# Performance work log

Hardware: AMD Instinct MI355X
Metric: run time of the kernel (lower is better)

## Reference

```python
import jax, jax.numpy as jnp
import numpy as np

IN_CH = 256
BOT = IN_CH // 2  # bottleneck channels
B, W, H = 4, 64, 64


def setup_inputs() -> dict:
    key = jax.random.key(0)
    ks = jax.random.split(key, 10)
    s_in = 1.0 / np.sqrt(IN_CH)   # torch Conv2d default init scale (kaiming-ish bound)
    s_bt = 1.0 / np.sqrt(BOT)
    return {
        "X": jax.random.normal(ks[0], (B, IN_CH, W, H), dtype=jnp.float32),
        "Wq": jax.random.uniform(ks[1], (BOT, IN_CH), jnp.float32, -s_in, s_in),
        "bq": jax.random.uniform(ks[2], (BOT,), jnp.float32, -s_in, s_in),
        "Wk": jax.random.uniform(ks[3], (BOT, IN_CH), jnp.float32, -s_in, s_in),
        "bk": jax.random.uniform(ks[4], (BOT,), jnp.float32, -s_in, s_in),
        "Wv": jax.random.uniform(ks[5], (BOT, IN_CH), jnp.float32, -s_in, s_in),
        "bv": jax.random.uniform(ks[6], (BOT,), jnp.float32, -s_in, s_in),
        "Wo": jax.random.uniform(ks[7], (IN_CH, BOT), jnp.float32, -s_bt, s_bt),
        "bo": jax.random.uniform(ks[8], (IN_CH,), jnp.float32, -s_bt, s_bt),
        "gamma": 0.1 * jax.random.normal(ks[9], (1,), dtype=jnp.float32),
    }


def reference(X, Wq, bq, Wk, bk, Wv, bv, Wo, bo, gamma):
    b, c, w, h = X.shape
    n = w * h
    Xf = X.reshape(b, c, n)  # [b, c, n] — 1x1 conv == per-pixel linear
    q = jnp.einsum('oc,bcn->bon', Wq, Xf) + bq[None, :, None]  # [b, c/2, n]
    k = jnp.einsum('oc,bcn->bon', Wk, Xf) + bk[None, :, None]
    v = jnp.einsum('oc,bcn->bon', Wv, Xf) + bv[None, :, None]
    # score[b,i,j] = sum_c q[b,c,i] * k[b,c,j]; softmax over dim=1 (query index i)
    score = jnp.einsum('bci,bcj->bij', q, k)          # [b, n, n]
    attn = jax.nn.softmax(score, axis=1)
    out = jnp.einsum('bci,bij->bcj', v, attn)         # [b, c/2, n]
    out = jnp.einsum('oc,bcn->bon', Wo, out) + bo[None, :, None]  # [b, c, n]
    out = out.reshape(b, c, w, h)
    return gamma[0] * out + X
```

## Files before the change

### kernel.cpp

```cpp
#include <hip/hip_runtime.h>
#include <math.h>

#define NBATCH 4
#define CIN    256
#define CBOT   128
#define NPIX   4096
#define NPART  4
#define LOG2E  1.44269504f

typedef __attribute__((ext_vector_type(4))) float f32x4;
typedef __attribute__((ext_vector_type(8))) short bf16x8;

__device__ __forceinline__ unsigned short f2bf(float f) {
    union { float f; unsigned u; } v; v.f = f;
    unsigned r = (v.u + 0x7FFFu + ((v.u >> 16) & 1u)) >> 16;
    return (unsigned short)r;
}

__global__ __launch_bounds__(256) void k_wcvt(
    const float* __restrict__ Wq, const float* __restrict__ Wk,
    const float* __restrict__ Wv, const float* __restrict__ Wo,
    unsigned short* __restrict__ Wb)
{
    const int f4 = (blockIdx.x * 256 + threadIdx.x) * 4;
    const int reg = f4 >> 15, loc = f4 & 32767;
    const float* __restrict__ W = (reg == 0) ? Wq : (reg == 1) ? Wk : (reg == 2) ? Wv : Wo;
    const float sc = (reg == 1) ? LOG2E : 1.f;
    float4 v = *(const float4*)(W + loc);
    ushort4 u;
    u.x = f2bf(v.x * sc); u.y = f2bf(v.y * sc);
    u.z = f2bf(v.z * sc); u.w = f2bf(v.w * sc);
    *(ushort4*)&Wb[f4] = u;
}

__global__ __launch_bounds__(256) void k_xt(
    const float* __restrict__ X, unsigned short* __restrict__ Xt)
{
    __shared__ float T[64][65];
    const int tid = threadIdx.x;
    const int pbase = blockIdx.x * 64;
    const int c0    = blockIdx.y * 64;
    const int b     = blockIdx.z;
#pragma unroll
    for (int k = 0; k < 4; ++k) {
        int f = tid + 256 * k;
        int cl = f >> 4, p4 = (f & 15) << 2;
        float4 v = *(const float4*)(X + (size_t)b * CIN * NPIX + (size_t)(c0 + cl) * NPIX + pbase + p4);
        T[cl][p4 + 0] = v.x; T[cl][p4 + 1] = v.y;
        T[cl][p4 + 2] = v.z; T[cl][p4 + 3] = v.w;
    }
    __syncthreads();
#pragma unroll
    for (int k = 0; k < 4; ++k) {
        int f = tid + 256 * k;
        int p = f >> 4, c4 = (f & 15) << 2;
        ushort4 u;
        u.x = f2bf(T[c4 + 0][p]); u.y = f2bf(T[c4 + 1][p]);
        u.z = f2bf(T[c4 + 2][p]); u.w = f2bf(T[c4 + 3][p]);
        *(ushort4*)&Xt[((size_t)b * NPIX + pbase + p) * CIN + c0 + c4] = u;
    }
}

__global__ __launch_bounds__(256) void k_qkv(
    const unsigned short* __restrict__ Xt,
    const unsigned short* __restrict__ Wb,
    const float* __restrict__ bq, const float* __restrict__ bk,
    const float* __restrict__ bv,
    unsigned short* __restrict__ Qt, unsigned short* __restrict__ Kt,
    unsigned short* __restrict__ Vt)
{
    const int tid = threadIdx.x;
    const int wv = tid >> 6, lane = tid & 63;
    const int grp = lane & 15, quad = lane >> 4;
    const int pbase = blockIdx.x * 32;
    const int b     = blockIdx.y;
    const unsigned short* __restrict__ Xb  = Xt + (size_t)b * NPIX * CIN;
    const unsigned short* __restrict__ Wqb = Wb;
    const unsigned short* __restrict__ Wkb = Wb + 32768;
    const unsigned short* __restrict__ Wvb = Wb + 65536;
    const int obase = 32 * wv;

    f32x4 aQ[2][2], aK[2][2], aV[2][2];
#pragma unroll
    for (int mt = 0; mt < 2; ++mt)
#pragma unroll
        for (int nt = 0; nt < 2; ++nt) {
            aQ[mt][nt] = (f32x4)0.f; aK[mt][nt] = (f32x4)0.f; aV[mt][nt] = (f32x4)0.f;
        }

    for (int ks = 0; ks < 8; ++ks) {
        bf16x8 bx[2];
#pragma unroll
        for (int nt = 0; nt < 2; ++nt)
            bx[nt] = *(const bf16x8*)&Xb[(size_t)(pbase + nt * 16 + grp) * CIN + ks * 32 + quad * 8];
        bf16x8 wq_[2], wk_[2], wv_[2];
#pragma unroll
        for (int mt = 0; mt < 2; ++mt) {
            const size_t roff = (size_t)(obase + mt * 16 + grp) * CIN + ks * 32 + quad * 8;
            wq_[mt] = *(const bf16x8*)&Wqb[roff];
            wk_[mt] = *(const bf16x8*)&Wkb[roff];
            wv_[mt] = *(const bf16x8*)&Wvb[roff];
        }
#pragma unroll
        for (int mt = 0; mt < 2; ++mt)
#pragma unroll
            for (int nt = 0; nt < 2; ++nt) {
                aQ[mt][nt] = __builtin_amdgcn_mfma_f32_16x16x32_bf16(wq_[mt], bx[nt], aQ[mt][nt], 0, 0, 0);
                aK[mt][nt] = __builtin_amdgcn_mfma_f32_16x16x32_bf16(wk_[mt], bx[nt], aK[mt][nt], 0, 0, 0);
                aV[mt][nt] = __builtin_amdgcn_mfma_f32_16x16x32_bf16(bx[mt], wv_[nt], aV[mt][nt], 0, 0, 0);
            }
    }

    unsigned short* Qb_ = Qt + (size_t)b * NPIX * CBOT;
    unsigned short* Kb_ = Kt + (size_t)b * NPIX * CBOT;
#pragma unroll
    for (int mt = 0; mt < 2; ++mt) {
        int o0 = obase + mt * 16 + quad * 4;
        float b4q[4], b4k[4];
#pragma unroll
        for (int r = 0; r < 4; ++r) { b4q[r] = bq[o0 + r]; b4k[r] = bk[o0 + r] * LOG2E; }
#pragma unroll
        for (int nt = 0; nt < 2; ++nt) {
            int p = pbase + nt * 16 + grp;
            ushort4 uq, uk;
            uq.x = f2bf(aQ[mt][nt][0] + b4q[0]); uq.y = f2bf(aQ[mt][nt][1] + b4q[1]);
            uq.z = f2bf(aQ[mt][nt][2] + b4q[2]); uq.w = f2bf(aQ[mt][nt][3] + b4q[3]);
            uk.x = f2bf(aK[mt][nt][0] + b4k[0]); uk.y = f2bf(aK[mt][nt][1] + b4k[1]);
            uk.z = f2bf(aK[mt][nt][2] + b4k[2]); uk.w = f2bf(aK[mt][nt][3] + b4k[3]);
            *(ushort4*)&Qb_[(size_t)p * CBOT + o0] = uq;
            *(ushort4*)&Kb_[(size_t)p * CBOT + o0] = uk;
        }
    }
    unsigned short* Vb_ = Vt + (size_t)b * CBOT * NPIX;
#pragma unroll
    for (int nt = 0; nt < 2; ++nt) {
        int o = obase + nt * 16 + grp;
        float bb = bv[o];
#pragma unroll
        for (int mt = 0; mt < 2; ++mt) {
            int p0 = pbase + mt * 16 + quad * 4;
            ushort4 u;
            u.x = f2bf(aV[mt][nt][0] + bb); u.y = f2bf(aV[mt][nt][1] + bb);
            u.z = f2bf(aV[mt][nt][2] + bb); u.w = f2bf(aV[mt][nt][3] + bb);
            *(ushort4*)&Vb_[(size_t)o * NPIX + p0] = u;
        }
    }
}

__global__ __launch_bounds__(256, 2) void k_flash(
    const unsigned short* __restrict__ Qt,
    const unsigned short* __restrict__ Kt,
    const unsigned short* __restrict__ Vt,
    unsigned short* __restrict__ Opart,
    float* __restrict__ Lpart)
{
    __shared__ __align__(16) unsigned short Qs[64][136];
    __shared__ __align__(16) unsigned short Vs[128][72];
    __shared__ __align__(16) unsigned short Ps[128][72];
    const int tid  = threadIdx.x;
    const int wv   = tid >> 6, lane = tid & 63;
    const int grp  = lane & 15, quad = lane >> 4;
    const int jblk = blockIdx.x * 128;
    const int part = blockIdx.y;
    const int b    = blockIdx.z;
    const int tbeg = part * (64 / NPART);
    const int tend = tbeg + (64 / NPART);
    const unsigned short* __restrict__ Qb = Qt + (size_t)b * NPIX * CBOT;
    const unsigned short* __restrict__ Kb = Kt + (size_t)b * NPIX * CBOT;
    const unsigned short* __restrict__ Vb = Vt + (size_t)b * CBOT * NPIX;

    bf16x8 aq[2][4];
#pragma unroll
    for (int set = 0; set < 2; ++set)
#pragma unroll
        for (int ks = 0; ks < 4; ++ks)
            aq[set][ks] = *(const bf16x8*)&Kb[
                (size_t)(jblk + wv * 32 + set * 16 + grp) * CBOT + ks * 32 + quad * 8];

    bf16x8 bones;
#pragma unroll
    for (int t = 0; t < 8; ++t) bones[t] = (short)0x3F80;

    f32x4 o[2][8];
#pragma unroll
    for (int set = 0; set < 2; ++set)
#pragma unroll
        for (int ct = 0; ct < 8; ++ct) o[set][ct] = (f32x4)0.f;
    f32x4 lacc[2] = {(f32x4)0.f, (f32x4)0.f};

    const int qrow = tid >> 4, qch = tid & 15;
    const int vrow = tid >> 3, vch = tid & 7;
    bf16x8 qreg[4], vreg[4];
#pragma unroll
    for (int k = 0; k < 4; ++k) {
        qreg[k] = *(const bf16x8*)&Qb[(size_t)(tbeg * 64 + qrow + 16 * k) * CBOT + qch * 8];
        vreg[k] = *(const bf16x8*)&Vb[(size_t)(vrow + 32 * k) * NPIX + tbeg * 64 + vch * 8];
    }

    for (int it = tbeg; it < tend; ++it) {
        __syncthreads();
#pragma unroll
        for (int k = 0; k < 4; ++k) {
            *(bf16x8*)&Qs[qrow + 16 * k][qch * 8] = qreg[k];
            *(bf16x8*)&Vs[vrow + 32 * k][vch * 8] = vreg[k];
        }
        __syncthreads();
        if (it + 1 < tend) {
            const int i1 = (it + 1) * 64;
#pragma unroll
            for (int k = 0; k < 4; ++k) {
                qreg[k] = *(const bf16x8*)&Qb[(size_t)(i1 + qrow + 16 * k) * CBOT + qch * 8];
                vreg[k] = *(const bf16x8*)&Vb[(size_t)(vrow + 32 * k) * NPIX + i1 + vch * 8];
            }
        }

        f32x4 sf[2][4];
#pragma unroll
        for (int set = 0; set < 2; ++set)
#pragma unroll
            for (int nt = 0; nt < 4; ++nt) sf[set][nt] = (f32x4)0.f;
#pragma unroll
        for (int nt = 0; nt < 4; ++nt)
#pragma unroll
            for (int ks = 0; ks < 4; ++ks) {
                bf16x8 bq_ = *(const bf16x8*)&Qs[nt * 16 + grp][ks * 32 + quad * 8];
                sf[0][nt] = __builtin_amdgcn_mfma_f32_16x16x32_bf16(aq[0][ks], bq_, sf[0][nt], 0, 0, 0);
                sf[1][nt] = __builtin_amdgcn_mfma_f32_16x16x32_bf16(aq[1][ks], bq_, sf[1][nt], 0, 0, 0);
            }

#pragma unroll
        for (int set = 0; set < 2; ++set)
#pragma unroll
            for (int nt = 0; nt < 4; ++nt)
#pragma unroll
                for (int r = 0; r < 4; ++r)
                    Ps[wv * 32 + set * 16 + quad * 4 + r][nt * 16 + grp] =
                        f2bf(exp2f(sf[set][nt][r]));

        bf16x8 af[2][2];
#pragma unroll
        for (int set = 0; set < 2; ++set)
#pragma unroll
            for (int ks2 = 0; ks2 < 2; ++ks2)
                af[set][ks2] = *(const bf16x8*)&Ps[wv * 32 + set * 16 + grp][ks2 * 32 + quad * 8];

#pragma unroll
        for (int ct = 0; ct < 8; ++ct)
#pragma unroll
            for (int ks2 = 0; ks2 < 2; ++ks2) {
                bf16x8 bv_ = *(const bf16x8*)&Vs[ct * 16 + grp][ks2 * 32 + quad * 8];
                o[0][ct] = __builtin_amdgcn_mfma_f32_16x16x32_bf16(af[0][ks2], bv_, o[0][ct], 0, 0, 0);
                o[1][ct] = __builtin_amdgcn_mfma_f32_16x16x32_bf16(af[1][ks2], bv_, o[1][ct], 0, 0, 0);
            }
#pragma unroll
        for (int set = 0; set < 2; ++set) {
            lacc[set] = __builtin_amdgcn_mfma_f32_16x16x32_bf16(af[set][0], bones, lacc[set], 0, 0, 0);
            lacc[set] = __builtin_amdgcn_mfma_f32_16x16x32_bf16(af[set][1], bones, lacc[set], 0, 0, 0);
        }
    }

    unsigned short* Ob = Opart + ((size_t)(part * NBATCH + b) * NPIX + jblk) * CBOT;
#pragma unroll
    for (int set = 0; set < 2; ++set)
#pragma unroll
        for (int ct = 0; ct < 8; ++ct)
#pragma unroll
            for (int r = 0; r < 4; ++r)
                Ob[(size_t)(wv * 32 + set * 16 + quad * 4 + r) * CBOT + ct * 16 + grp] =
                    f2bf(o[set][ct][r]);
    if (grp == 0) {
#pragma unroll
        for (int set = 0; set < 2; ++set)
#pragma unroll
            for (int r = 0; r < 4; ++r)
                Lpart[(size_t)(part * NBATCH + b) * NPIX + jblk + wv * 32 + set * 16 + quad * 4 + r] =
                    lacc[set][r];
    }
}

__global__ __launch_bounds__(256) void k_oproj(
    const unsigned short* __restrict__ Opart, const float* __restrict__ Lpart,
    const unsigned short* __restrict__ Wob, const float* __restrict__ bo,
    const float* __restrict__ gamma, const float* __restrict__ X,
    float* __restrict__ Out)
{
    const int tid = threadIdx.x;
    const int wv = tid >> 6, lane = tid & 63;
    const int grp = lane & 15, quad = lane >> 4;
    const int pbase = blockIdx.x * 32;
    const int b     = blockIdx.y;
    const int obase = 64 * wv;

    f32x4 acc[2][4];
#pragma unroll
    for (int mt = 0; mt < 2; ++mt)
#pragma unroll
        for (int nt = 0; nt < 4; ++nt) acc[mt][nt] = (f32x4)0.f;

    for (int ks = 0; ks < 4; ++ks) {
        bf16x8 bw[4];
#pragma unroll
        for (int nt = 0; nt < 4; ++nt)
            bw[nt] = *(const bf16x8*)&Wob[(size_t)(obase + nt * 16 + grp) * CBOT + ks * 32 + quad * 8];
#pragma unroll
        for (int mt = 0; mt < 2; ++mt) {
            int p = pbase + mt * 16 + grp;
#pragma unroll
            for (int part = 0; part < NPART; ++part) {
                bf16x8 ao = *(const bf16x8*)&Opart[
                    ((size_t)(part * NBATCH + b) * NPIX + p) * CBOT + ks * 32 + quad * 8];
#pragma unroll
                for (int nt = 0; nt < 4; ++nt)
                    acc[mt][nt] = __builtin_amdgcn_mfma_f32_16x16x32_bf16(ao, bw[nt], acc[mt][nt], 0, 0, 0);
            }
        }
    }

    float linv[2][4];
#pragma unroll
    for (int mt = 0; mt < 2; ++mt)
#pragma unroll
        for (int r = 0; r < 4; ++r) {
            int p = pbase + mt * 16 + quad * 4 + r;
            float ls = 0.f;
#pragma unroll
            for (int part = 0; part < NPART; ++part)
                ls += Lpart[(size_t)(part * NBATCH + b) * NPIX + p];
            linv[mt][r] = 1.f / ls;
        }
    float g = gamma[0];
#pragma unroll
    for (int nt = 0; nt < 4; ++nt) {
        int o = obase + nt * 16 + grp;
        float bb = bo[o];
#pragma unroll
        for (int mt = 0; mt < 2; ++mt) {
            int p0 = pbase + mt * 16 + quad * 4;
            size_t base = (size_t)b * CIN * NPIX + (size_t)o * NPIX + p0;
            float4 x4 = *(const float4*)(X + base);
            float4 r4;
            r4.x = g * (acc[mt][nt][0] * linv[mt][0] + bb) + x4.x;
            r4.y = g * (acc[mt][nt][1] * linv[mt][1] + bb) + x4.y;
            r4.z = g * (acc[mt][nt][2] * linv[mt][2] + bb) + x4.z;
            r4.w = g * (acc[mt][nt][3] * linv[mt][3] + bb) + x4.w;
            *(float4*)(Out + base) = r4;
        }
    }
}

extern "C" void kernel_launch(void* const* d_in, const int* in_sizes, int n_in,
                              void* d_out, int out_size, void* d_ws, size_t ws_size,
                              hipStream_t stream)
{
    (void)in_sizes; (void)n_in; (void)out_size; (void)ws_size;
    const float* X     = (const float*)d_in[0];
    const float* Wq    = (const float*)d_in[1];
    const float* bq    = (const float*)d_in[2];
    const float* Wk    = (const float*)d_in[3];
    const float* bk    = (const float*)d_in[4];
    const float* Wv    = (const float*)d_in[5];
    const float* bv    = (const float*)d_in[6];
    const float* Wo    = (const float*)d_in[7];
    const float* bo    = (const float*)d_in[8];
    const float* gamma = (const float*)d_in[9];
    float* out = (float*)d_out;

    const size_t BNC = (size_t)NBATCH * NPIX * CBOT;
    unsigned short* Qt    = (unsigned short*)d_ws;
    unsigned short* Kt    = Qt + BNC;
    unsigned short* Vt    = Kt + BNC;
    unsigned short* Opart = Vt + BNC;
    unsigned short* Xt    = Opart;
    float*          Lpart = (float*)(Opart + (size_t)NPART * BNC);
    unsigned short* Wb    = (unsigned short*)(Lpart + (size_t)NPART * NBATCH * NPIX);

    k_wcvt <<<dim3(128),               256, 0, stream>>>(Wq, Wk, Wv, Wo, Wb);
    k_xt   <<<dim3(64, 4, NBATCH),     256, 0, stream>>>(X, Xt);
    k_qkv  <<<dim3(128, NBATCH),       256, 0, stream>>>(Xt, Wb, bq, bk, bv, Qt, Kt, Vt);
    k_flash<<<dim3(32, NPART, NBATCH), 256, 0, stream>>>(Qt, Kt, Vt, Opart, Lpart);
    k_oproj<<<dim3(128, NBATCH),       256, 0, stream>>>(Opart, Lpart, Wb + 98304, bo, gamma, X, out);
}
```

Baseline: 174.5 us.

## Merge prep kernels, raise flash split count and occupancy, pack bf16 conversions

```diff
diff --git a/kernel.cpp b/kernel.cpp
--- a/kernel.cpp
+++ b/kernel.cpp
@@ -5,7 +5,6 @@
 #define CIN    256
 #define CBOT   128
 #define NPIX   4096
-#define NPART  4
 #define LOG2E  1.44269504f
 
 typedef __attribute__((ext_vector_type(4))) float f32x4;
@@ -16,28 +15,56 @@
     unsigned r = (v.u + 0x7FFFu + ((v.u >> 16) & 1u)) >> 16;
     return (unsigned short)r;
 }
-
-__global__ __launch_bounds__(256) void k_wcvt(
+__device__ __forceinline__ unsigned pk2bf(float a, float b) {
+#if __has_builtin(__builtin_amdgcn_cvt_pk_bf16_f32)
+    auto r = __builtin_amdgcn_cvt_pk_bf16_f32(a, b);
+    unsigned u; __builtin_memcpy(&u, &r, 4); return u;
+#else
+    return (unsigned)f2bf(a) | ((unsigned)f2bf(b) << 16);
+#endif
+}
+__device__ __forceinline__ float fexp2(float x) {
+#if __has_builtin(__builtin_amdgcn_exp2f)
+    return __builtin_amdgcn_exp2f(x);
+#else
+    return exp2f(x);
+#endif
+}
+
+__global__ __launch_bounds__(256) void k_prep(
+    const float* __restrict__ X,
     const float* __restrict__ Wq, const float* __restrict__ Wk,
     const float* __restrict__ Wv, const float* __restrict__ Wo,
-    unsigned short* __restrict__ Wb)
-{
-    const int f4 = (blockIdx.x * 256 + threadIdx.x) * 4;
-    const int reg = f4 >> 15, loc = f4 & 32767;
-    const float* __restrict__ W = (reg == 0) ? Wq : (reg == 1) ? Wk : (reg == 2) ? Wv : Wo;
-    const float sc = (reg == 1) ? LOG2E : 1.f;
-    float4 v = *(const float4*)(W + loc);
-    ushort4 u;
-    u.x = f2bf(v.x * sc); u.y = f2bf(v.y * sc);
-    u.z = f2bf(v.z * sc); u.w = f2bf(v.w * sc);
-    *(ushort4*)&Wb[f4] = u;
-}
-
-__global__ __launch_bounds__(256) void k_xt(
-    const float* __restrict__ X, unsigned short* __restrict__ Xt)
+    unsigned short* __restrict__ Xt, unsigned short* __restrict__ Wb)
 {
     __shared__ float T[64][65];
     const int tid = threadIdx.x;
+    if (blockIdx.y == 4) {
+        const int gid = blockIdx.z * 64 + blockIdx.x;
+        if (gid < 128) {
+            const int f4 = (gid * 256 + tid) * 4;
+            const int reg = f4 >> 15, loc = f4 & 32767;
+            if (reg < 3) {
+                const float* __restrict__ W = (reg == 0) ? Wq : (reg == 1) ? Wk : Wv;
+                const float sc = (reg == 1) ? LOG2E : 1.f;
+                float4 v = *(const float4*)(W + loc);
+                uint2 u;
+                u.x = pk2bf(v.x * sc, v.y * sc);
+                u.y = pk2bf(v.z * sc, v.w * sc);
+                *(uint2*)&Wb[f4] = u;
+            } else {
+                const int o = loc >> 7, s0 = loc & 127;
+                const int k = s0 >> 3, cb = s0 & 7;
+                float w0 = Wo[o * CBOT + (cb + 0) * 16 + k];
+                float w1 = Wo[o * CBOT + (cb + 1) * 16 + k];
+                float w2 = Wo[o * CBOT + (cb + 2) * 16 + k];
+                float w3 = Wo[o * CBOT + (cb + 3) * 16 + k];
+                uint2 u; u.x = pk2bf(w0, w1); u.y = pk2bf(w2, w3);
+                *(uint2*)&Wb[f4] = u;
+            }
+        }
+        return;
+    }
     const int pbase = blockIdx.x * 64;
     const int c0    = blockIdx.y * 64;
     const int b     = blockIdx.z;
@@ -54,10 +81,10 @@
     for (int k = 0; k < 4; ++k) {
         int f = tid + 256 * k;
         int p = f >> 4, c4 = (f & 15) << 2;
-        ushort4 u;
-        u.x = f2bf(T[c4 + 0][p]); u.y = f2bf(T[c4 + 1][p]);
-        u.z = f2bf(T[c4 + 2][p]); u.w = f2bf(T[c4 + 3][p]);
-        *(ushort4*)&Xt[((size_t)b * NPIX + pbase + p) * CIN + c0 + c4] = u;
+        uint2 u;
+        u.x = pk2bf(T[c4 + 0][p], T[c4 + 1][p]);
+        u.y = pk2bf(T[c4 + 2][p], T[c4 + 3][p]);
+        *(uint2*)&Xt[((size_t)b * NPIX + pbase + p) * CIN + c0 + c4] = u;
     }
 }
 
@@ -122,13 +149,13 @@
 #pragma unroll
         for (int nt = 0; nt < 2; ++nt) {
             int p = pbase + nt * 16 + grp;
-            ushort4 uq, uk;
-            uq.x = f2bf(aQ[mt][nt][0] + b4q[0]); uq.y = f2bf(aQ[mt][nt][1] + b4q[1]);
-            uq.z = f2bf(aQ[mt][nt][2] + b4q[2]); uq.w = f2bf(aQ[mt][nt][3] + b4q[3]);
-            uk.x = f2bf(aK[mt][nt][0] + b4k[0]); uk.y = f2bf(aK[mt][nt][1] + b4k[1]);
-            uk.z = f2bf(aK[mt][nt][2] + b4k[2]); uk.w = f2bf(aK[mt][nt][3] + b4k[3]);
-            *(ushort4*)&Qb_[(size_t)p * CBOT + o0] = uq;
-            *(ushort4*)&Kb_[(size_t)p * CBOT + o0] = uk;
+            uint2 uq, uk;
+            uq.x = pk2bf(aQ[mt][nt][0] + b4q[0], aQ[mt][nt][1] + b4q[1]);
+            uq.y = pk2bf(aQ[mt][nt][2] + b4q[2], aQ[mt][nt][3] + b4q[3]);
+            uk.x = pk2bf(aK[mt][nt][0] + b4k[0], aK[mt][nt][1] + b4k[1]);
+            uk.y = pk2bf(aK[mt][nt][2] + b4k[2], aK[mt][nt][3] + b4k[3]);
+            *(uint2*)&Qb_[(size_t)p * CBOT + o0] = uq;
+            *(uint2*)&Kb_[(size_t)p * CBOT + o0] = uk;
         }
     }
     unsigned short* Vb_ = Vt + (size_t)b * CBOT * NPIX;
@@ -139,32 +166,32 @@
 #pragma unroll
         for (int mt = 0; mt < 2; ++mt) {
             int p0 = pbase + mt * 16 + quad * 4;
-            ushort4 u;
-            u.x = f2bf(aV[mt][nt][0] + bb); u.y = f2bf(aV[mt][nt][1] + bb);
-            u.z = f2bf(aV[mt][nt][2] + bb); u.w = f2bf(aV[mt][nt][3] + bb);
-            *(ushort4*)&Vb_[(size_t)o * NPIX + p0] = u;
-        }
-    }
-}
-
-__global__ __launch_bounds__(256, 2) void k_flash(
+            uint2 u;
+            u.x = pk2bf(aV[mt][nt][0] + bb, aV[mt][nt][1] + bb);
+            u.y = pk2bf(aV[mt][nt][2] + bb, aV[mt][nt][3] + bb);
+            *(uint2*)&Vb_[(size_t)o * NPIX + p0] = u;
+        }
+    }
+}
+
+__global__ __launch_bounds__(256, 3) void k_flash(
     const unsigned short* __restrict__ Qt,
     const unsigned short* __restrict__ Kt,
     const unsigned short* __restrict__ Vt,
     unsigned short* __restrict__ Opart,
-    float* __restrict__ Lpart)
+    float* __restrict__ Lpart, int npart)
 {
-    __shared__ __align__(16) unsigned short Qs[64][136];
-    __shared__ __align__(16) unsigned short Vs[128][72];
-    __shared__ __align__(16) unsigned short Ps[128][72];
+    __shared__ __align__(16) unsigned short Qs[64][132];
+    __shared__ __align__(16) unsigned short Vs[128][68];
+    __shared__ __align__(16) unsigned short Ps[128][68];
     const int tid  = threadIdx.x;
     const int wv   = tid >> 6, lane = tid & 63;
     const int grp  = lane & 15, quad = lane >> 4;
     const int jblk = blockIdx.x * 128;
     const int part = blockIdx.y;
     const int b    = blockIdx.z;
-    const int tbeg = part * (64 / NPART);
-    const int tend = tbeg + (64 / NPART);
+    const int tbeg = (part * 64) / npart;
+    const int tend = ((part + 1) * 64) / npart;
     const unsigned short* __restrict__ Qb = Qt + (size_t)b * NPIX * CBOT;
     const unsigned short* __restrict__ Kb = Kt + (size_t)b * NPIX * CBOT;
     const unsigned short* __restrict__ Vb = Vt + (size_t)b * CBOT * NPIX;
@@ -229,13 +256,19 @@
             }
 
 #pragma unroll
-        for (int set = 0; set < 2; ++set)
-#pragma unroll
-            for (int nt = 0; nt < 4; ++nt)
-#pragma unroll
-                for (int r = 0; r < 4; ++r)
-                    Ps[wv * 32 + set * 16 + quad * 4 + r][nt * 16 + grp] =
-                        f2bf(exp2f(sf[set][nt][r]));
+        for (int set = 0; set < 2; ++set) {
+            const int rbase = wv * 32 + set * 16 + quad * 4;
+#pragma unroll
+            for (int nt = 0; nt < 4; ++nt) {
+                const int col = nt * 16 + grp;
+                unsigned u01 = pk2bf(fexp2(sf[set][nt][0]), fexp2(sf[set][nt][1]));
+                unsigned u23 = pk2bf(fexp2(sf[set][nt][2]), fexp2(sf[set][nt][3]));
+                Ps[rbase + 0][col] = (unsigned short)u01;
+                Ps[rbase + 1][col] = (unsigned short)(u01 >> 16);
+                Ps[rbase + 2][col] = (unsigned short)u23;
+                Ps[rbase + 3][col] = (unsigned short)(u23 >> 16);
+            }
+        }
 
         bf16x8 af[2][2];
 #pragma unroll
@@ -263,11 +296,15 @@
 #pragma unroll
     for (int set = 0; set < 2; ++set)
 #pragma unroll
-        for (int ct = 0; ct < 8; ++ct)
-#pragma unroll
-            for (int r = 0; r < 4; ++r)
-                Ob[(size_t)(wv * 32 + set * 16 + quad * 4 + r) * CBOT + ct * 16 + grp] =
-                    f2bf(o[set][ct][r]);
+        for (int r = 0; r < 4; ++r) {
+            const int row = wv * 32 + set * 16 + quad * 4 + r;
+            uint4 u;
+            u.x = pk2bf(o[set][0][r], o[set][1][r]);
+            u.y = pk2bf(o[set][2][r], o[set][3][r]);
+            u.z = pk2bf(o[set][4][r], o[set][5][r]);
+            u.w = pk2bf(o[set][6][r], o[set][7][r]);
+            *(uint4*)&Ob[(size_t)row * CBOT + grp * 8] = u;
+        }
     if (grp == 0) {
 #pragma unroll
         for (int set = 0; set < 2; ++set)
@@ -282,7 +319,7 @@
     const unsigned short* __restrict__ Opart, const float* __restrict__ Lpart,
     const unsigned short* __restrict__ Wob, const float* __restrict__ bo,
     const float* __restrict__ gamma, const float* __restrict__ X,
-    float* __restrict__ Out)
+    float* __restrict__ Out, int npart)
 {
     const int tid = threadIdx.x;
     const int wv = tid >> 6, lane = tid & 63;
@@ -305,8 +342,7 @@
 #pragma unroll
         for (int mt = 0; mt < 2; ++mt) {
             int p = pbase + mt * 16 + grp;
-#pragma unroll
-            for (int part = 0; part < NPART; ++part) {
+            for (int part = 0; part < npart; ++part) {
                 bf16x8 ao = *(const bf16x8*)&Opart[
                     ((size_t)(part * NBATCH + b) * NPIX + p) * CBOT + ks * 32 + quad * 8];
 #pragma unroll
@@ -323,8 +359,7 @@
         for (int r = 0; r < 4; ++r) {
             int p = pbase + mt * 16 + quad * 4 + r;
             float ls = 0.f;
-#pragma unroll
-            for (int part = 0; part < NPART; ++part)
+            for (int part = 0; part < npart; ++part)
                 ls += Lpart[(size_t)(part * NBATCH + b) * NPIX + p];
             linv[mt][r] = 1.f / ls;
         }
@@ -352,7 +387,7 @@
                               void* d_out, int out_size, void* d_ws, size_t ws_size,
                               hipStream_t stream)
 {
-    (void)in_sizes; (void)n_in; (void)out_size; (void)ws_size;
+    (void)in_sizes; (void)n_in; (void)out_size;
     const float* X     = (const float*)d_in[0];
     const float* Wq    = (const float*)d_in[1];
     const float* bq    = (const float*)d_in[2];
@@ -369,14 +404,15 @@
     unsigned short* Qt    = (unsigned short*)d_ws;
     unsigned short* Kt    = Qt + BNC;
     unsigned short* Vt    = Kt + BNC;
-    unsigned short* Opart = Vt + BNC;
+    float*          Lpart = (float*)(Vt + BNC);
+    unsigned short* Wb    = (unsigned short*)(Lpart + (size_t)6 * NBATCH * NPIX);
+    unsigned short* Opart = Wb + 131072;
     unsigned short* Xt    = Opart;
-    float*          Lpart = (float*)(Opart + (size_t)NPART * BNC);
-    unsigned short* Wb    = (unsigned short*)(Lpart + (size_t)NPART * NBATCH * NPIX);
-
-    k_wcvt <<<dim3(128),               256, 0, stream>>>(Wq, Wk, Wv, Wo, Wb);
-    k_xt   <<<dim3(64, 4, NBATCH),     256, 0, stream>>>(X, Xt);
-    k_qkv  <<<dim3(128, NBATCH),       256, 0, stream>>>(Xt, Wb, bq, bk, bv, Qt, Kt, Vt);
-    k_flash<<<dim3(32, NPART, NBATCH), 256, 0, stream>>>(Qt, Kt, Vt, Opart, Lpart);
-    k_oproj<<<dim3(128, NBATCH),       256, 0, stream>>>(Opart, Lpart, Wb + 98304, bo, gamma, X, out);
-}
+    const size_t base_bytes = (size_t)((char*)Opart - (char*)d_ws);
+    const int npart = (ws_size >= base_bytes + 6 * BNC * 2) ? 6 : 4;
+
+    k_prep <<<dim3(64, 5, NBATCH),      256, 0, stream>>>(X, Wq, Wk, Wv, Wo, Xt, Wb);
+    k_qkv  <<<dim3(128, NBATCH),        256, 0, stream>>>(Xt, Wb, bq, bk, bv, Qt, Kt, Vt);
+    k_flash<<<dim3(32, npart, NBATCH),  256, 0, stream>>>(Qt, Kt, Vt, Opart, Lpart, npart);
+    k_oproj<<<dim3(128, NBATCH),        256, 0, stream>>>(Opart, Lpart, Wb + 98304, bo, gamma, X, out, npart);
+}
```

New measurement: 197.8 us. +13.4%, slower.
